# Kernel optimization log

Hardware: AMD Instinct MI355X
Metric: run time of the kernel (lower is better)

The kernel has to match this reference:

```python
import jax, jax.numpy as jnp
import numpy as np

B = 8192
ND, NS, NF = 13, 26, 39          # dense feats, sparse feats, seq_len
E, H, HD = 64, 8, 8              # embed_dim, heads, head_dim
L = 4                            # num_layers
FF = 4 * E                       # 256 mlp hidden
HID = 256                        # output head hidden
VD, VS = 50, 50000               # vocab sizes
SCALE = HD ** -0.5
EPS = 1e-5


def setup_inputs() -> dict:
    key = jax.random.key(0)
    ks = iter(jax.random.split(key, 32))
    n = lambda shape, s=0.02: jax.random.normal(next(ks), shape, jnp.float32) * s
    inp = {
        "dense_feats": jax.random.randint(next(ks), (B, ND), 0, VD),
        "sparse_feats": jax.random.randint(next(ks), (B, NS), 0, VS),
        "dense_emb": n((ND, VD, E)),
        "sparse_emb": n((NS, VS, E)),
        # per-layer params stacked on leading L axis (for lax.scan)
        "wq": n((L, E, E)), "bq": jnp.zeros((L, E)),
        "wk": n((L, E, E)), "bk": jnp.zeros((L, E)),
        "wv": n((L, E, E)), "bv": jnp.zeros((L, E)),
        "wo": n((L, E, E)), "bo": jnp.zeros((L, E)),
        "ln1_g": jnp.ones((L, E)), "ln1_b": jnp.zeros((L, E)),
        "ln2_g": jnp.ones((L, E)), "ln2_b": jnp.zeros((L, E)),
        "mlp_w1": n((L, E, FF)), "mlp_b1": jnp.zeros((L, FF)),
        "mlp_w2": n((L, FF, E)), "mlp_b2": jnp.zeros((L, E)),
        "out_w1": n((E * NF, HID)), "out_b1": jnp.zeros((HID,)),
        "out_w2": n((HID, 1)), "out_b2": jnp.zeros((1,)),
    }
    return inp


def _layernorm(x, g, b):
    m = jnp.mean(x, -1, keepdims=True)
    v = jnp.var(x, -1, keepdims=True)
    return (x - m) * jax.lax.rsqrt(v + EPS) * g + b


def _block(x, p):
    (wq, bq, wk, bk, wv, bv, wo, bo, g1, be1, g2, be2, w1, b1, w2, b2) = p
    h = _layernorm(x, g1, be1)
    bsz = h.shape[0]
    q = (h @ wq + bq).reshape(bsz, NF, H, HD)
    k = (h @ wk + bk).reshape(bsz, NF, H, HD)
    v = (h @ wv + bv).reshape(bsz, NF, H, HD)
    attn = jax.nn.sigmoid(jnp.einsum('bqhd,bkhd->bhqk', q, k) * SCALE)
    o = jnp.einsum('bhqk,bkhd->bqhd', attn, v).reshape(bsz, NF, E)
    x = x + (o @ wo + bo)
    h2 = _layernorm(x, g2, be2)
    x = x + (jax.nn.gelu(h2 @ w1 + b1) @ w2 + b2)
    return x, None


def reference(dense_feats, sparse_feats, dense_emb, sparse_emb,
              wq, bq, wk, bk, wv, bv, wo, bo,
              ln1_g, ln1_b, ln2_g, ln2_b,
              mlp_w1, mlp_b1, mlp_w2, mlp_b2,
              out_w1, out_b1, out_w2, out_b2):
    # 39-way embedding gather -> [B, 39, E]
    de = dense_emb[jnp.arange(ND)[None, :], dense_feats]    # [B,13,E]
    se = sparse_emb[jnp.arange(NS)[None, :], sparse_feats]  # [B,26,E]
    x = jnp.concatenate([de, se], axis=1)
    params = (wq, bq, wk, bk, wv, bv, wo, bo,
              ln1_g, ln1_b, ln2_g, ln2_b, mlp_w1, mlp_b1, mlp_w2, mlp_b2)
    x, _ = jax.lax.scan(_block, x, params)
    flat = x.reshape(x.shape[0], -1)                        # [B, 39*E]
    h = jax.nn.relu(flat @ out_w1 + out_b1)
    return jax.nn.sigmoid(h @ out_w2 + out_b2)[:, 0]        # [B]
```

## Files before the change

kernel.cpp:

```cpp
#include <hip/hip_runtime.h>
#include <hip/hip_bf16.h>

#define NDENSE 13
#define NSPARSE 26
#define NFEAT 39
#define EDIM 64
#define NLAYER 4
#define FFDIM 256
#define VDN 50
#define VSN 50000
#define NSAMP 8192
#define LN_EPS 1e-5f

#define QSCL 0.5100697f
#define GC1 2.3022082f
#define GC2 0.10294324f

#define XST 72
#define QST 72
#define VST 104
#define FST 264

#define OFF_XB 0
#define OFF_QB 11520
#define OFF_KB 25344
#define OFF_VT 39168
#define SMEM_TOTAL 52480
#define OFF_FF OFF_KB

#define FLATX_ELEMS (8192L * NFEAT * EDIM)
#define PK_WKT 4096
#define PK_WVT 8192
#define PK_WOT 12288
#define PK_W1T 16384
#define PK_W2T 32768
#define PK_LAYER 49152
#define PK_OW1T 196608
#define PK_TOTAL 835584

typedef __bf16 bf16x8 __attribute__((ext_vector_type(8)));
typedef __bf16 bf16x4 __attribute__((ext_vector_type(4)));
typedef float f32x4 __attribute__((ext_vector_type(4)));
typedef int int32x4 __attribute__((ext_vector_type(4)));

__device__ __forceinline__ f32x4 mfma16(bf16x8 a, bf16x8 b, f32x4 c) {
    return __builtin_amdgcn_mfma_f32_16x16x32_bf16(a, b, c, 0, 0, 0);
}

__device__ __forceinline__ float exp2_fast(float x) {
#if __has_builtin(__builtin_amdgcn_exp2f)
    return __builtin_amdgcn_exp2f(x);
#else
    return exp2f(x);
#endif
}
__device__ __forceinline__ float sigmoid2(float x) {
    return __builtin_amdgcn_rcpf(1.0f + exp2_fast(-x));
}
__device__ __forceinline__ float gelu_f(float x) {
    return x * sigmoid2(GC1 * x + GC2 * x * x * x);
}

__device__ __forceinline__ bf16x8 ldfrag(const __bf16* WT, int ld, int col, int k0) {
    return *(const bf16x8*)&WT[col * ld + k0];
}
__device__ __forceinline__ bf16x4 pk4(f32x4 v) {
    bf16x4 r; r[0]=(__bf16)v[0]; r[1]=(__bf16)v[1]; r[2]=(__bf16)v[2]; r[3]=(__bf16)v[3]; return r;
}
__device__ __forceinline__ int pk2(float a, float b) {
    unsigned short ua = __builtin_bit_cast(unsigned short, (__bf16)a);
    unsigned short ub = __builtin_bit_cast(unsigned short, (__bf16)b);
    return (int)(((unsigned)ub << 16) | (unsigned)ua);
}
__device__ __forceinline__ void rmw4(__bf16* p, f32x4 a) {
    bf16x4 o = *(bf16x4*)p;
    f32x4 n = { (float)o[0]+a[0], (float)o[1]+a[1], (float)o[2]+a[2], (float)o[3]+a[3] };
    *(bf16x4*)p = pk4(n);
}
__device__ __forceinline__ int xrow(int q48) {
    int s = q48 >= 48 ? 1 : 0;
    int ql = q48 - 48 * s;
    if (ql > 39) ql = 39;
    return 40 * s + ql;
}

__device__ __forceinline__ void ln_frag(const __bf16* xr, const float* gam, const float* bet,
                                        int g, bf16x8& a0, bf16x8& a1) {
    bf16x8 v0 = *(const bf16x8*)(xr + g * 8);
    bf16x8 v1 = *(const bf16x8*)(xr + 32 + g * 8);
    float x0[8], x1[8], s = 0.f, ss = 0.f;
    #pragma unroll
    for (int j = 0; j < 8; ++j) {
        x0[j] = (float)v0[j]; x1[j] = (float)v1[j];
        s += x0[j] + x1[j];
        ss += x0[j] * x0[j] + x1[j] * x1[j];
    }
    s += __shfl_xor(s, 16); ss += __shfl_xor(ss, 16);
    s += __shfl_xor(s, 32); ss += __shfl_xor(ss, 32);
    float mn = s * (1.0f / 64.0f);
    float rs = rsqrtf(ss * (1.0f / 64.0f) - mn * mn + LN_EPS);
    float gv0[8], gv1[8], bv0[8], bv1[8];
    *(f32x4*)&gv0[0] = *(const f32x4*)&gam[g * 8];
    *(f32x4*)&gv0[4] = *(const f32x4*)&gam[g * 8 + 4];
    *(f32x4*)&gv1[0] = *(const f32x4*)&gam[32 + g * 8];
    *(f32x4*)&gv1[4] = *(const f32x4*)&gam[32 + g * 8 + 4];
    *(f32x4*)&bv0[0] = *(const f32x4*)&bet[g * 8];
    *(f32x4*)&bv0[4] = *(const f32x4*)&bet[g * 8 + 4];
    *(f32x4*)&bv1[0] = *(const f32x4*)&bet[32 + g * 8];
    *(f32x4*)&bv1[4] = *(const f32x4*)&bet[32 + g * 8 + 4];
    #pragma unroll
    for (int j = 0; j < 8; ++j) {
        a0[j] = (__bf16)((x0[j] - mn) * rs * gv0[j] + bv0[j]);
        a1[j] = (__bf16)((x1[j] - mn) * rs * gv1[j] + bv1[j]);
    }
}

__global__ __launch_bounds__(256)
void pack_weights(const float* __restrict__ wq, const float* __restrict__ wk,
                  const float* __restrict__ wv, const float* __restrict__ wo,
                  const float* __restrict__ w1, const float* __restrict__ w2,
                  const float* __restrict__ ow1, __bf16* __restrict__ pk)
{
    int idx = blockIdx.x * 256 + threadIdx.x;
    if (idx >= PK_TOTAL) return;
    float v;
    if (idx < PK_OW1T) {
        int l = idx / PK_LAYER, r = idx - l * PK_LAYER;
        const float* src; int sh, N, off;
        if (r < PK_WKT)      { src = wq + l * 4096;  sh = 6; N = 64;  off = r; }
        else if (r < PK_WVT) { src = wk + l * 4096;  sh = 6; N = 64;  off = r - PK_WKT; }
        else if (r < PK_WOT) { src = wv + l * 4096;  sh = 6; N = 64;  off = r - PK_WVT; }
        else if (r < PK_W1T) { src = wo + l * 4096;  sh = 6; N = 64;  off = r - PK_WOT; }
        else if (r < PK_W2T) { src = w1 + l * 16384; sh = 6; N = 256; off = r - PK_W1T; }
        else                 { src = w2 + l * 16384; sh = 8; N = 64;  off = r - PK_W2T; }
        int col = off >> sh, k = off & ((1 << sh) - 1);
        v = src[k * N + col];
    } else {
        int off = idx - PK_OW1T;
        int col = off / 2496, k = off - col * 2496;
        v = ow1[k * 256 + col];
    }
    pk[idx] = (__bf16)v;
}

__global__ __launch_bounds__(256, 3)
void hstu_fused(const int* __restrict__ dfeat, const int* __restrict__ sfeat,
                const float* __restrict__ demb, const float* __restrict__ semb,
                const float* __restrict__ bq, const float* __restrict__ bk,
                const float* __restrict__ bv, const float* __restrict__ bo,
                const float* __restrict__ ln1g, const float* __restrict__ ln1b,
                const float* __restrict__ ln2g, const float* __restrict__ ln2b,
                const float* __restrict__ b1, const float* __restrict__ b2,
                const __bf16* __restrict__ pk, __bf16* __restrict__ flatX)
{
    __shared__ __align__(16) char smem[SMEM_TOTAL];
    __bf16* xb = (__bf16*)(smem + OFF_XB);
    __bf16* Qb = (__bf16*)(smem + OFF_QB);
    __bf16* Kb = (__bf16*)(smem + OFF_KB);
    __bf16* Vt = (__bf16*)(smem + OFF_VT);
    __bf16* ff = (__bf16*)(smem + OFF_FF);

    const int tid = threadIdx.x;
    const int lane = tid & 63, w = tid >> 6;
    const int g = lane >> 4, r16 = lane & 15;
    const int s0 = blockIdx.x * 2;

    for (int r = w; r < 80; r += 4) {
        int sm = r / 40, f = r % 40;
        float val = 0.0f;
        if (f < NFEAT) {
            if (f < NDENSE) {
                int idx = dfeat[(s0 + sm) * NDENSE + f];
                val = demb[(f * VDN + idx) * EDIM + lane];
            } else {
                int idx = sfeat[(s0 + sm) * NSPARSE + (f - NDENSE)];
                val = semb[((long)(f - NDENSE) * VSN + idx) * EDIM + lane];
            }
        }
        xb[r * XST + lane] = (__bf16)val;
    }
    __syncthreads();

    for (int lay = 0; lay < NLAYER; ++lay) {
        const __bf16* wqT = pk + lay * PK_LAYER;
        const __bf16* wkT = wqT + PK_WKT;
        const __bf16* wvT = wqT + PK_WVT;
        const __bf16* woT = wqT + PK_WOT;
        const __bf16* w1T = wqT + PK_W1T;
        const __bf16* w2T = wqT + PK_W2T;
        const float* bq_l = bq + lay * EDIM;
        const float* bk_l = bk + lay * EDIM;
        const float* bv_l = bv + lay * EDIM;
        const float* bo_l = bo + lay * EDIM;
        const float* g1_l = ln1g + lay * EDIM;
        const float* be1_l = ln1b + lay * EDIM;
        const float* g2_l = ln2g + lay * EDIM;
        const float* be2_l = ln2b + lay * EDIM;
        const float* b1_l = b1 + lay * FFDIM;
        const float* b2_l = b2 + lay * EDIM;

        {
            bf16x8 lnB[6][2];
            #pragma unroll
            for (int t = 0; t < 6; ++t)
                ln_frag(&xb[xrow(16 * t + r16) * XST], g1_l, be1_l, g, lnB[t][0], lnB[t][1]);

            const __bf16* Wm[3] = { wqT, wkT, wvT };
            const float*  Bm[3] = { bq_l, bk_l, bv_l };
            #pragma unroll
            for (int m = 0; m < 3; ++m) {
                bf16x8 A0 = ldfrag(Wm[m], EDIM, 16 * w + r16, 8 * g);
                bf16x8 A1 = ldfrag(Wm[m], EDIM, 16 * w + r16, 32 + 8 * g);
                f32x4 bi4 = *(const f32x4*)&Bm[m][16 * w + 4 * g];
                #pragma unroll
                for (int t = 0; t < 6; ++t) {
                    f32x4 acc = bi4;
                    acc = mfma16(A0, lnB[t][0], acc);
                    acc = mfma16(A1, lnB[t][1], acc);
                    int q48 = 16 * t + r16;
                    if (m == 0) {
                        f32x4 sc = { acc[0]*QSCL, acc[1]*QSCL, acc[2]*QSCL, acc[3]*QSCL };
                        *(bf16x4*)&Qb[q48 * QST + 16 * w + 4 * g] = pk4(sc);
                    } else if (m == 1) {
                        *(bf16x4*)&Kb[q48 * QST + 16 * w + 4 * g] = pk4(acc);
                    } else {
                        bool vz = ((t % 3) * 16 + r16) >= 39;
                        #pragma unroll
                        for (int r = 0; r < 4; ++r)
                            Vt[(16 * w + 4 * g + r) * VST + q48] =
                                vz ? (__bf16)0.0f : (__bf16)acc[r];
                    }
                }
            }
        }
        __syncthreads();

        #pragma unroll
        for (int s = 0; s < 2; ++s) {
            int sp[2][3][3][2];
            {
                bf16x8 qf[3], kf[3];
                #pragma unroll
                for (int hh = 0; hh < 2; ++hh) {
                    const int h = 2 * w + hh;
                    #pragma unroll
                    for (int t = 0; t < 3; ++t) {
                        bf16x8 z = {};
                        qf[t] = z; kf[t] = z;
                        if (g == 0) {
                            qf[t] = *(const bf16x8*)&Qb[(48*s + 16*t + r16) * QST + 8*h];
                            kf[t] = *(const bf16x8*)&Kb[(48*s + 16*t + r16) * QST + 8*h];
                        }
                    }
                    #pragma unroll
                    for (int kt = 0; kt < 3; ++kt) {
                        #pragma unroll
                        for (int qt = 0; qt < 3; ++qt) {
                            f32x4 acc = {0.f, 0.f, 0.f, 0.f};
                            acc = mfma16(kf[kt], qf[qt], acc);
                            sp[hh][kt][qt][0] = pk2(sigmoid2(acc[0]), sigmoid2(acc[1]));
                            sp[hh][kt][qt][1] = pk2(sigmoid2(acc[2]), sigmoid2(acc[3]));
                        }
                    }
                }
            }
            f32x4 oacc[3];
            {
                f32x4 z = {0.f, 0.f, 0.f, 0.f};
                oacc[0] = z; oacc[1] = z; oacc[2] = z;
            }
            {
                const int sAh[3] = {0,0,1}, sAt[3] = {0,2,1};
                const int sBh[3] = {0,1,1}, sBt[3] = {1,0,2};
                const int l0 = ((lane & 16) << 1) + r16;
                const int l1 = l0 + 16;
                const bool selA = (g < 2);
                #pragma unroll
                for (int ks = 0; ks < 3; ++ks) {
                    int slot0 = 32 * ks + 8 * g;
                    int side = slot0 >= 48 ? 1 : 0;
                    int kk0 = slot0 - 48 * side;
                    bf16x8 av = {};
                    if (side == (r16 >> 3))
                        av = *(const bf16x8*)&Vt[(16 * w + r16) * VST + 48 * s + kk0];
                    #pragma unroll
                    for (int qt = 0; qt < 3; ++qt) {
                        int a0 = sp[sAh[ks]][sAt[ks]][qt][0];
                        int a1 = sp[sAh[ks]][sAt[ks]][qt][1];
                        int b0 = sp[sBh[ks]][sBt[ks]][qt][0];
                        int b1 = sp[sBh[ks]][sBt[ks]][qt][1];
                        int va0 = __shfl(a0, l0), va1 = __shfl(a1, l0);
                        int va2 = __shfl(a0, l1), va3 = __shfl(a1, l1);
                        int vb0 = __shfl(b0, l0), vb1 = __shfl(b1, l0);
                        int vb2 = __shfl(b0, l1), vb3 = __shfl(b1, l1);
                        int32x4 bi = { selA ? va0 : vb0, selA ? va1 : vb1,
                                       selA ? va2 : vb2, selA ? va3 : vb3 };
                        oacc[qt] = mfma16(av, __builtin_bit_cast(bf16x8, bi), oacc[qt]);
                    }
                }
            }
            #pragma unroll
            for (int qt = 0; qt < 3; ++qt) {
                int q48 = 48 * s + 16 * qt + r16;
                *(bf16x4*)&Qb[q48 * QST + 16 * w + 4 * g] = pk4(oacc[qt]);
            }
        }
        __syncthreads();

        {
            bf16x8 A0 = ldfrag(woT, EDIM, 16 * w + r16, 8 * g);
            bf16x8 A1 = ldfrag(woT, EDIM, 16 * w + r16, 32 + 8 * g);
            f32x4 bo4 = *(const f32x4*)&bo_l[16 * w + 4 * g];
            #pragma unroll
            for (int t = 0; t < 6; ++t) {
                bf16x8 B0 = *(const bf16x8*)&Qb[(16 * t + r16) * QST + 8 * g];
                bf16x8 B1 = *(const bf16x8*)&Qb[(16 * t + r16) * QST + 32 + 8 * g];
                f32x4 acc = bo4;
                acc = mfma16(A0, B0, acc);
                acc = mfma16(A1, B1, acc);
                int ql = (t % 3) * 16 + r16;
                if (ql <= 39)
                    rmw4(&xb[(40 * (t / 3) + ql) * XST + 16 * w + 4 * g], acc);
            }
        }
        __syncthreads();

        #pragma unroll
        for (int p = 0; p < 2; ++p) {
            bf16x8 ln2B[3][2];
            #pragma unroll
            for (int tt = 0; tt < 3; ++tt)
                ln_frag(&xb[xrow(48 * p + 16 * tt + r16) * XST], g2_l, be2_l, g,
                        ln2B[tt][0], ln2B[tt][1]);
            #pragma unroll
            for (int ft = 0; ft < 4; ++ft) {
                int m = 4 * w + ft;
                bf16x8 A0 = ldfrag(w1T, EDIM, 16 * m + r16, 8 * g);
                bf16x8 A1 = ldfrag(w1T, EDIM, 16 * m + r16, 32 + 8 * g);
                f32x4 b14 = *(const f32x4*)&b1_l[16 * m + 4 * g];
                #pragma unroll
                for (int tt = 0; tt < 3; ++tt) {
                    f32x4 acc = b14;
                    acc = mfma16(A0, ln2B[tt][0], acc);
                    acc = mfma16(A1, ln2B[tt][1], acc);
                    f32x4 gl = { gelu_f(acc[0]), gelu_f(acc[1]),
                                 gelu_f(acc[2]), gelu_f(acc[3]) };
                    *(bf16x4*)&ff[(16 * tt + r16) * FST + 16 * m + 4 * g] = pk4(gl);
                }
            }
            __syncthreads();
            {
                f32x4 b24 = *(const f32x4*)&b2_l[16 * w + 4 * g];
                #pragma unroll
                for (int tt = 0; tt < 3; ++tt) {
                    f32x4 acc = b24;
                    #pragma unroll
                    for (int kf = 0; kf < 8; ++kf) {
                        bf16x8 Af = ldfrag(w2T, FFDIM, 16 * w + r16, 32 * kf + 8 * g);
                        bf16x8 Bf = *(const bf16x8*)&ff[(16 * tt + r16) * FST + 32 * kf + 8 * g];
                        acc = mfma16(Af, Bf, acc);
                    }
                    int ql = 16 * tt + r16;
                    if (ql <= 39)
                        rmw4(&xb[(40 * p + ql) * XST + 16 * w + 4 * g], acc);
                }
            }
            __syncthreads();
        }
    }

    for (int r = w; r < 80; r += 4) {
        int sm = r / 40, f = r % 40;
        if (f < NFEAT)
            flatX[((long)(s0 + sm) * NFEAT + f) * EDIM + lane] = xb[r * XST + lane];
    }
}

#define FFSTH 264
__global__ __launch_bounds__(512)
void final_mlp(const __bf16* __restrict__ flatX, const __bf16* __restrict__ ow1T,
               const float* __restrict__ ob1, const float* __restrict__ ow2,
               const float* __restrict__ ob2, float* __restrict__ out)
{
    __shared__ __bf16 hbuf[32 * FFSTH];
    const int tid = threadIdx.x, lane = tid & 63, wave = tid >> 6;
    const int g = lane >> 4, r16 = lane & 15;
    const int m = wave & 1;
    const long base = (long)blockIdx.x * 32;
    const long arow = (base + m * 16 + r16) * (long)(NFEAT * EDIM);

    f32x4 acc[4];
    #pragma unroll
    for (int i = 0; i < 4; ++i) {
        int n = (wave >> 1) + i * 4;
        float bz = ob1[n * 16 + r16];
        f32x4 t = {bz, bz, bz, bz};
        acc[i] = t;
    }
    for (int kf = 0; kf < 78; ++kf) {
        bf16x8 af = *(const bf16x8*)&flatX[arow + kf * 32 + g * 8];
        #pragma unroll
        for (int i = 0; i < 4; ++i) {
            int n = (wave >> 1) + i * 4;
            bf16x8 bfr = ldfrag(ow1T, NFEAT * EDIM, n * 16 + r16, kf * 32 + g * 8);
            acc[i] = mfma16(af, bfr, acc[i]);
        }
    }
    #pragma unroll
    for (int i = 0; i < 4; ++i) {
        int n = (wave >> 1) + i * 4;
        #pragma unroll
        for (int r = 0; r < 4; ++r) {
            float h = acc[i][r];
            hbuf[(m * 16 + g * 4 + r) * FFSTH + n * 16 + r16] = (__bf16)(h > 0.f ? h : 0.f);
        }
    }
    __syncthreads();
    float w2v0 = ow2[lane], w2v1 = ow2[64 + lane], w2v2 = ow2[128 + lane], w2v3 = ow2[192 + lane];
    float bias2 = ob2[0];
    #pragma unroll
    for (int i = 0; i < 4; ++i) {
        int sm = wave * 4 + i;
        float part = (float)hbuf[sm * FFSTH + lane]       * w2v0
                   + (float)hbuf[sm * FFSTH + 64 + lane]  * w2v1
                   + (float)hbuf[sm * FFSTH + 128 + lane] * w2v2
                   + (float)hbuf[sm * FFSTH + 192 + lane] * w2v3;
        #pragma unroll
        for (int off = 32; off >= 1; off >>= 1) part += __shfl_xor(part, off);
        if (lane == 0) {
            float z = part + bias2;
            out[base + sm] = __builtin_amdgcn_rcpf(1.0f + __expf(-z));
        }
    }
}

extern "C" void kernel_launch(void* const* d_in, const int* in_sizes, int n_in,
                              void* d_out, int out_size, void* d_ws, size_t ws_size,
                              hipStream_t stream)
{
    const int*   dfeat = (const int*)d_in[0];
    const int*   sfeat = (const int*)d_in[1];
    const float* demb  = (const float*)d_in[2];
    const float* semb  = (const float*)d_in[3];
    const float* wq    = (const float*)d_in[4];
    const float* bq    = (const float*)d_in[5];
    const float* wk    = (const float*)d_in[6];
    const float* bk    = (const float*)d_in[7];
    const float* wv    = (const float*)d_in[8];
    const float* bv    = (const float*)d_in[9];
    const float* wo    = (const float*)d_in[10];
    const float* bo    = (const float*)d_in[11];
    const float* ln1g  = (const float*)d_in[12];
    const float* ln1b  = (const float*)d_in[13];
    const float* ln2g  = (const float*)d_in[14];
    const float* ln2b  = (const float*)d_in[15];
    const float* w1    = (const float*)d_in[16];
    const float* b1    = (const float*)d_in[17];
    const float* w2    = (const float*)d_in[18];
    const float* b2    = (const float*)d_in[19];
    const float* ow1   = (const float*)d_in[20];
    const float* ob1   = (const float*)d_in[21];
    const float* ow2   = (const float*)d_in[22];
    const float* ob2   = (const float*)d_in[23];

    __bf16* flatX = (__bf16*)d_ws;
    __bf16* pk    = ((__bf16*)d_ws) + FLATX_ELEMS;
    float* out = (float*)d_out;

    pack_weights<<<(PK_TOTAL + 255) / 256, 256, 0, stream>>>(wq, wk, wv, wo, w1, w2, ow1, pk);
    hstu_fused<<<NSAMP / 2, 256, 0, stream>>>(dfeat, sfeat, demb, semb,
        bq, bk, bv, bo, ln1g, ln1b, ln2g, ln2b, b1, b2, pk, flatX);
    final_mlp<<<NSAMP / 32, 512, 0, stream>>>(flatX, pk + PK_OW1T, ob1, ow2, ob2, out);
}
```

Baseline: 806.2 us.

## Double waves per block and redistribute transformer stages across eight waves

The fused transformer kernel moves from 4 to 8 waves per block. Waves now split work by sample half and output column tile, and attention computes QK tiles on the fly per k-step instead of keeping all sigmoid scores in registers. LN2 is now computed once into shared memory (reusing the V region) rather than recomputed per wave, and the MLP up/down projections are spread across the 8 waves. The goal is more latency hiding and lower register pressure per wave. The cost is extra barriers, and the 12-unit down-projection loop leaves some waves idle.

```diff
diff --git a/kernel.cpp b/kernel.cpp
--- a/kernel.cpp
+++ b/kernel.cpp
@@ -26,7 +26,8 @@
 #define OFF_KB 25344
 #define OFF_VT 39168
 #define SMEM_TOTAL 52480
-#define OFF_FF OFF_KB
+#define OFF_FF OFF_QB
+#define OFF_LNS OFF_VT
 
 #define FLATX_ELEMS (8192L * NFEAT * EDIM)
 #define PK_WKT 4096
@@ -112,6 +113,22 @@
     for (int j = 0; j < 8; ++j) {
         a0[j] = (__bf16)((x0[j] - mn) * rs * gv0[j] + bv0[j]);
         a1[j] = (__bf16)((x1[j] - mn) * rs * gv1[j] + bv1[j]);
+    }
+}
+
+__device__ __forceinline__ void qk_tile(const __bf16* Qb, const __bf16* Kb,
+                                        int s, int h, int kt, int g, int r16,
+                                        int sp[3][2]) {
+    bf16x8 kf = {};
+    if (g == 0) kf = *(const bf16x8*)&Kb[(48*s + 16*kt + r16) * QST + 8*h];
+    #pragma unroll
+    for (int qt = 0; qt < 3; ++qt) {
+        bf16x8 qf = {};
+        if (g == 0) qf = *(const bf16x8*)&Qb[(48*s + 16*qt + r16) * QST + 8*h];
+        f32x4 acc = {0.f, 0.f, 0.f, 0.f};
+        acc = mfma16(kf, qf, acc);
+        sp[qt][0] = pk2(sigmoid2(acc[0]), sigmoid2(acc[1]));
+        sp[qt][1] = pk2(sigmoid2(acc[2]), sigmoid2(acc[3]));
     }
 }
 
@@ -143,7 +160,7 @@
     pk[idx] = (__bf16)v;
 }
 
-__global__ __launch_bounds__(256, 3)
+__global__ __launch_bounds__(512, 6)
 void hstu_fused(const int* __restrict__ dfeat, const int* __restrict__ sfeat,
                 const float* __restrict__ demb, const float* __restrict__ semb,
                 const float* __restrict__ bq, const float* __restrict__ bk,
@@ -154,18 +171,21 @@
                 const __bf16* __restrict__ pk, __bf16* __restrict__ flatX)
 {
     __shared__ __align__(16) char smem[SMEM_TOTAL];
-    __bf16* xb = (__bf16*)(smem + OFF_XB);
-    __bf16* Qb = (__bf16*)(smem + OFF_QB);
-    __bf16* Kb = (__bf16*)(smem + OFF_KB);
-    __bf16* Vt = (__bf16*)(smem + OFF_VT);
-    __bf16* ff = (__bf16*)(smem + OFF_FF);
+    __bf16* xb  = (__bf16*)(smem + OFF_XB);
+    __bf16* Qb  = (__bf16*)(smem + OFF_QB);
+    __bf16* Kb  = (__bf16*)(smem + OFF_KB);
+    __bf16* Vt  = (__bf16*)(smem + OFF_VT);
+    __bf16* ff  = (__bf16*)(smem + OFF_FF);
+    __bf16* LNS = (__bf16*)(smem + OFF_LNS);
 
     const int tid = threadIdx.x;
     const int lane = tid & 63, w = tid >> 6;
     const int g = lane >> 4, r16 = lane & 15;
+    const int oc = w & 3;
+    const int th = w >> 2;
     const int s0 = blockIdx.x * 2;
 
-    for (int r = w; r < 80; r += 4) {
+    for (int r = w; r < 80; r += 8) {
         int sm = r / 40, f = r % 40;
         float val = 0.0f;
         if (f < NFEAT) {
@@ -200,34 +220,35 @@
         const float* b2_l = b2 + lay * EDIM;
 
         {
-            bf16x8 lnB[6][2];
+            bf16x8 lnB[3][2];
             #pragma unroll
-            for (int t = 0; t < 6; ++t)
-                ln_frag(&xb[xrow(16 * t + r16) * XST], g1_l, be1_l, g, lnB[t][0], lnB[t][1]);
+            for (int tt = 0; tt < 3; ++tt)
+                ln_frag(&xb[xrow(16 * (3*th + tt) + r16) * XST], g1_l, be1_l, g,
+                        lnB[tt][0], lnB[tt][1]);
 
             const __bf16* Wm[3] = { wqT, wkT, wvT };
             const float*  Bm[3] = { bq_l, bk_l, bv_l };
             #pragma unroll
             for (int m = 0; m < 3; ++m) {
-                bf16x8 A0 = ldfrag(Wm[m], EDIM, 16 * w + r16, 8 * g);
-                bf16x8 A1 = ldfrag(Wm[m], EDIM, 16 * w + r16, 32 + 8 * g);
-                f32x4 bi4 = *(const f32x4*)&Bm[m][16 * w + 4 * g];
+                bf16x8 A0 = ldfrag(Wm[m], EDIM, 16 * oc + r16, 8 * g);
+                bf16x8 A1 = ldfrag(Wm[m], EDIM, 16 * oc + r16, 32 + 8 * g);
+                f32x4 bi4 = *(const f32x4*)&Bm[m][16 * oc + 4 * g];
                 #pragma unroll
-                for (int t = 0; t < 6; ++t) {
+                for (int tt = 0; tt < 3; ++tt) {
                     f32x4 acc = bi4;
-                    acc = mfma16(A0, lnB[t][0], acc);
-                    acc = mfma16(A1, lnB[t][1], acc);
-                    int q48 = 16 * t + r16;
+                    acc = mfma16(A0, lnB[tt][0], acc);
+                    acc = mfma16(A1, lnB[tt][1], acc);
+                    int q48 = 16 * (3*th + tt) + r16;
                     if (m == 0) {
                         f32x4 sc = { acc[0]*QSCL, acc[1]*QSCL, acc[2]*QSCL, acc[3]*QSCL };
-                        *(bf16x4*)&Qb[q48 * QST + 16 * w + 4 * g] = pk4(sc);
+                        *(bf16x4*)&Qb[q48 * QST + 16 * oc + 4 * g] = pk4(sc);
                     } else if (m == 1) {
-                        *(bf16x4*)&Kb[q48 * QST + 16 * w + 4 * g] = pk4(acc);
+                        *(bf16x4*)&Kb[q48 * QST + 16 * oc + 4 * g] = pk4(acc);
                     } else {
-                        bool vz = ((t % 3) * 16 + r16) >= 39;
+                        bool vz = (16 * tt + r16) >= 39;
                         #pragma unroll
                         for (int r = 0; r < 4; ++r)
-                            Vt[(16 * w + 4 * g + r) * VST + q48] =
+                            Vt[(16 * oc + 4 * g + r) * VST + q48] =
                                 vz ? (__bf16)0.0f : (__bf16)acc[r];
                     }
                 }
@@ -235,141 +256,138 @@
         }
         __syncthreads();
 
-        #pragma unroll
-        for (int s = 0; s < 2; ++s) {
-            int sp[2][3][3][2];
-            {
-                bf16x8 qf[3], kf[3];
-                #pragma unroll
-                for (int hh = 0; hh < 2; ++hh) {
-                    const int h = 2 * w + hh;
-                    #pragma unroll
-                    for (int t = 0; t < 3; ++t) {
-                        bf16x8 z = {};
-                        qf[t] = z; kf[t] = z;
-                        if (g == 0) {
-                            qf[t] = *(const bf16x8*)&Qb[(48*s + 16*t + r16) * QST + 8*h];
-                            kf[t] = *(const bf16x8*)&Kb[(48*s + 16*t + r16) * QST + 8*h];
-                        }
-                    }
-                    #pragma unroll
-                    for (int kt = 0; kt < 3; ++kt) {
-                        #pragma unroll
-                        for (int qt = 0; qt < 3; ++qt) {
-                            f32x4 acc = {0.f, 0.f, 0.f, 0.f};
-                            acc = mfma16(kf[kt], qf[qt], acc);
-                            sp[hh][kt][qt][0] = pk2(sigmoid2(acc[0]), sigmoid2(acc[1]));
-                            sp[hh][kt][qt][1] = pk2(sigmoid2(acc[2]), sigmoid2(acc[3]));
-                        }
-                    }
-                }
-            }
+        {
+            const int s = th;
+            const int sAh[3] = {0,0,1}, sAt[3] = {0,2,1};
+            const int sBh[3] = {0,1,1}, sBt[3] = {1,0,2};
+            const int l0 = ((lane & 16) << 1) + r16;
+            const int l1 = l0 + 16;
+            const bool selA = (g < 2);
             f32x4 oacc[3];
             {
                 f32x4 z = {0.f, 0.f, 0.f, 0.f};
                 oacc[0] = z; oacc[1] = z; oacc[2] = z;
             }
-            {
-                const int sAh[3] = {0,0,1}, sAt[3] = {0,2,1};
-                const int sBh[3] = {0,1,1}, sBt[3] = {1,0,2};
-                const int l0 = ((lane & 16) << 1) + r16;
-                const int l1 = l0 + 16;
-                const bool selA = (g < 2);
+            #pragma unroll
+            for (int ks = 0; ks < 3; ++ks) {
+                int spA[3][2], spB[3][2];
+                qk_tile(Qb, Kb, s, 2*oc + sAh[ks], sAt[ks], g, r16, spA);
+                qk_tile(Qb, Kb, s, 2*oc + sBh[ks], sBt[ks], g, r16, spB);
+
+                int slot0 = 32 * ks + 8 * g;
+                int side = slot0 >= 48 ? 1 : 0;
+                int kk0 = slot0 - 48 * side;
+                bf16x8 av = {};
+                if (side == (r16 >> 3))
+                    av = *(const bf16x8*)&Vt[(16 * oc + r16) * VST + 48 * s + kk0];
                 #pragma unroll
-                for (int ks = 0; ks < 3; ++ks) {
-                    int slot0 = 32 * ks + 8 * g;
-                    int side = slot0 >= 48 ? 1 : 0;
-                    int kk0 = slot0 - 48 * side;
-                    bf16x8 av = {};
-                    if (side == (r16 >> 3))
-                        av = *(const bf16x8*)&Vt[(16 * w + r16) * VST + 48 * s + kk0];
-                    #pragma unroll
-                    for (int qt = 0; qt < 3; ++qt) {
-                        int a0 = sp[sAh[ks]][sAt[ks]][qt][0];
-                        int a1 = sp[sAh[ks]][sAt[ks]][qt][1];
-                        int b0 = sp[sBh[ks]][sBt[ks]][qt][0];
-                        int b1 = sp[sBh[ks]][sBt[ks]][qt][1];
-                        int va0 = __shfl(a0, l0), va1 = __shfl(a1, l0);
-                        int va2 = __shfl(a0, l1), va3 = __shfl(a1, l1);
-                        int vb0 = __shfl(b0, l0), vb1 = __shfl(b1, l0);
-                        int vb2 = __shfl(b0, l1), vb3 = __shfl(b1, l1);
-                        int32x4 bi = { selA ? va0 : vb0, selA ? va1 : vb1,
-                                       selA ? va2 : vb2, selA ? va3 : vb3 };
-                        oacc[qt] = mfma16(av, __builtin_bit_cast(bf16x8, bi), oacc[qt]);
-                    }
+                for (int qt = 0; qt < 3; ++qt) {
+                    int a0 = spA[qt][0], a1 = spA[qt][1];
+                    int b0 = spB[qt][0], b1 = spB[qt][1];
+                    int va0 = __shfl(a0, l0), va1 = __shfl(a1, l0);
+                    int va2 = __shfl(a0, l1), va3 = __shfl(a1, l1);
+                    int vb0 = __shfl(b0, l0), vb1 = __shfl(b1, l0);
+                    int vb2 = __shfl(b0, l1), vb3 = __shfl(b1, l1);
+                    int32x4 bi = { selA ? va0 : vb0, selA ? va1 : vb1,
+                                   selA ? va2 : vb2, selA ? va3 : vb3 };
+                    oacc[qt] = mfma16(av, __builtin_bit_cast(bf16x8, bi), oacc[qt]);
                 }
             }
             #pragma unroll
             for (int qt = 0; qt < 3; ++qt) {
                 int q48 = 48 * s + 16 * qt + r16;
-                *(bf16x4*)&Qb[q48 * QST + 16 * w + 4 * g] = pk4(oacc[qt]);
+                *(bf16x4*)&Qb[q48 * QST + 16 * oc + 4 * g] = pk4(oacc[qt]);
             }
         }
         __syncthreads();
 
         {
-            bf16x8 A0 = ldfrag(woT, EDIM, 16 * w + r16, 8 * g);
-            bf16x8 A1 = ldfrag(woT, EDIM, 16 * w + r16, 32 + 8 * g);
-            f32x4 bo4 = *(const f32x4*)&bo_l[16 * w + 4 * g];
+            bf16x8 A0 = ldfrag(woT, EDIM, 16 * oc + r16, 8 * g);
+            bf16x8 A1 = ldfrag(woT, EDIM, 16 * oc + r16, 32 + 8 * g);
+            f32x4 bo4 = *(const f32x4*)&bo_l[16 * oc + 4 * g];
             #pragma unroll
-            for (int t = 0; t < 6; ++t) {
+            for (int tt = 0; tt < 3; ++tt) {
+                int t = 3*th + tt;
                 bf16x8 B0 = *(const bf16x8*)&Qb[(16 * t + r16) * QST + 8 * g];
                 bf16x8 B1 = *(const bf16x8*)&Qb[(16 * t + r16) * QST + 32 + 8 * g];
                 f32x4 acc = bo4;
                 acc = mfma16(A0, B0, acc);
                 acc = mfma16(A1, B1, acc);
-                int ql = (t % 3) * 16 + r16;
+                int ql = 16 * tt + r16;
                 if (ql <= 39)
-                    rmw4(&xb[(40 * (t / 3) + ql) * XST + 16 * w + 4 * g], acc);
+                    rmw4(&xb[(40 * th + ql) * XST + 16 * oc + 4 * g], acc);
             }
         }
         __syncthreads();
 
-        #pragma unroll
         for (int p = 0; p < 2; ++p) {
-            bf16x8 ln2B[3][2];
-            #pragma unroll
-            for (int tt = 0; tt < 3; ++tt)
-                ln_frag(&xb[xrow(48 * p + 16 * tt + r16) * XST], g2_l, be2_l, g,
-                        ln2B[tt][0], ln2B[tt][1]);
-            #pragma unroll
-            for (int ft = 0; ft < 4; ++ft) {
-                int m = 4 * w + ft;
-                bf16x8 A0 = ldfrag(w1T, EDIM, 16 * m + r16, 8 * g);
-                bf16x8 A1 = ldfrag(w1T, EDIM, 16 * m + r16, 32 + 8 * g);
-                f32x4 b14 = *(const f32x4*)&b1_l[16 * m + 4 * g];
+            for (int u = w; u < 12; u += 8) {
+                int ql = 4 * u + g;
+                int qlc = ql > 39 ? 39 : ql;
+                bf16x4 v = *(const bf16x4*)&xb[(40 * p + qlc) * XST + 4 * r16];
+                float x0 = (float)v[0], x1 = (float)v[1], x2 = (float)v[2], x3 = (float)v[3];
+                float s = x0 + x1 + x2 + x3;
+                float ss = x0*x0 + x1*x1 + x2*x2 + x3*x3;
+                s += __shfl_xor(s, 1);  ss += __shfl_xor(ss, 1);
+                s += __shfl_xor(s, 2);  ss += __shfl_xor(ss, 2);
+                s += __shfl_xor(s, 4);  ss += __shfl_xor(ss, 4);
+                s += __shfl_xor(s, 8);  ss += __shfl_xor(ss, 8);
+                float mn = s * (1.0f / 64.0f);
+                float rs = rsqrtf(ss * (1.0f / 64.0f) - mn * mn + LN_EPS);
+                f32x4 gv = *(const f32x4*)&g2_l[4 * r16];
+                f32x4 bv = *(const f32x4*)&be2_l[4 * r16];
+                f32x4 nv = { (x0 - mn) * rs * gv[0] + bv[0],
+                             (x1 - mn) * rs * gv[1] + bv[1],
+                             (x2 - mn) * rs * gv[2] + bv[2],
+                             (x3 - mn) * rs * gv[3] + bv[3] };
+                *(bf16x4*)&LNS[ql * 72 + 4 * r16] = pk4(nv);
+            }
+            __syncthreads();
+
+            {
+                bf16x8 upB[3][2];
                 #pragma unroll
                 for (int tt = 0; tt < 3; ++tt) {
-                    f32x4 acc = b14;
-                    acc = mfma16(A0, ln2B[tt][0], acc);
-                    acc = mfma16(A1, ln2B[tt][1], acc);
-                    f32x4 gl = { gelu_f(acc[0]), gelu_f(acc[1]),
-                                 gelu_f(acc[2]), gelu_f(acc[3]) };
-                    *(bf16x4*)&ff[(16 * tt + r16) * FST + 16 * m + 4 * g] = pk4(gl);
+                    upB[tt][0] = *(const bf16x8*)&LNS[(16 * tt + r16) * 72 + 8 * g];
+                    upB[tt][1] = *(const bf16x8*)&LNS[(16 * tt + r16) * 72 + 32 + 8 * g];
                 }
+                #pragma unroll
+                for (int fi = 0; fi < 2; ++fi) {
+                    int ft = 2 * w + fi;
+                    bf16x8 A0 = ldfrag(w1T, EDIM, 16 * ft + r16, 8 * g);
+                    bf16x8 A1 = ldfrag(w1T, EDIM, 16 * ft + r16, 32 + 8 * g);
+                    f32x4 b14 = *(const f32x4*)&b1_l[16 * ft + 4 * g];
+                    #pragma unroll
+                    for (int tt = 0; tt < 3; ++tt) {
+                        f32x4 acc = b14;
+                        acc = mfma16(A0, upB[tt][0], acc);
+                        acc = mfma16(A1, upB[tt][1], acc);
+                        f32x4 gl = { gelu_f(acc[0]), gelu_f(acc[1]),
+                                     gelu_f(acc[2]), gelu_f(acc[3]) };
+                        *(bf16x4*)&ff[(16 * tt + r16) * FST + 16 * ft + 4 * g] = pk4(gl);
+                    }
+                }
             }
             __syncthreads();
-            {
-                f32x4 b24 = *(const f32x4*)&b2_l[16 * w + 4 * g];
+
+            for (int u = w; u < 12; u += 8) {
+                int oc2 = u & 3, tt = u >> 2;
+                f32x4 acc = *(const f32x4*)&b2_l[16 * oc2 + 4 * g];
                 #pragma unroll
-                for (int tt = 0; tt < 3; ++tt) {
-                    f32x4 acc = b24;
-                    #pragma unroll
-                    for (int kf = 0; kf < 8; ++kf) {
-                        bf16x8 Af = ldfrag(w2T, FFDIM, 16 * w + r16, 32 * kf + 8 * g);
-                        bf16x8 Bf = *(const bf16x8*)&ff[(16 * tt + r16) * FST + 32 * kf + 8 * g];
-                        acc = mfma16(Af, Bf, acc);
-                    }
-                    int ql = 16 * tt + r16;
-                    if (ql <= 39)
-                        rmw4(&xb[(40 * p + ql) * XST + 16 * w + 4 * g], acc);
+                for (int kf = 0; kf < 8; ++kf) {
+                    bf16x8 Af = ldfrag(w2T, FFDIM, 16 * oc2 + r16, 32 * kf + 8 * g);
+                    bf16x8 Bf = *(const bf16x8*)&ff[(16 * tt + r16) * FST + 32 * kf + 8 * g];
+                    acc = mfma16(Af, Bf, acc);
                 }
+                int ql = 16 * tt + r16;
+                if (ql <= 39)
+                    rmw4(&xb[(40 * p + ql) * XST + 16 * oc2 + 4 * g], acc);
             }
             __syncthreads();
         }
     }
 
-    for (int r = w; r < 80; r += 4) {
+    for (int r = w; r < 80; r += 8) {
         int sm = r / 40, f = r % 40;
         if (f < NFEAT)
             flatX[((long)(s0 + sm) * NFEAT + f) * EDIM + lane] = xb[r * XST + lane];
@@ -468,7 +486,7 @@
     float* out = (float*)d_out;
 
     pack_weights<<<(PK_TOTAL + 255) / 256, 256, 0, stream>>>(wq, wk, wv, wo, w1, w2, ow1, pk);
-    hstu_fused<<<NSAMP / 2, 256, 0, stream>>>(dfeat, sfeat, demb, semb,
+    hstu_fused<<<NSAMP / 2, 512, 0, stream>>>(dfeat, sfeat, demb, semb,
         bq, bk, bv, bo, ln1g, ln1b, ln2g, ln2b, b1, b2, pk, flatX);
     final_mlp<<<NSAMP / 32, 512, 0, stream>>>(flatX, pk + PK_OW1T, ob1, ow2, ob2, out);
 }
```

New measurement: 1.172 ms. 45.3% more time.
